# Optimization experiments

Hardware: AMD Instinct MI355X
Metric: run time of the kernel (lower is better)

The kernel has to match this reference:

```python
import jax, jax.numpy as jnp
import numpy as np

N = 65536  # number of points
# (out_ch, in_ch) for the 8 shared-MLP (1x1-conv) blocks
_DIMS = [(64, 3), (64, 64), (128, 64), (1024, 128), (512, 1088), (256, 512), (128, 256), (1, 128)]


def setup_inputs() -> dict:
    key = jax.random.key(0)
    ks = jax.random.split(key, 1 + 2 * len(_DIMS))
    inp = {"x": jax.random.normal(ks[0], (1, 1, N, 3), jnp.float32)}
    for i, (o, c) in enumerate(_DIMS):
        scale = 1.0 / np.sqrt(c)
        inp[f"W{i+1}"] = jax.random.normal(ks[1 + 2 * i], (o, c), jnp.float32) * scale
        inp[f"b{i+1}"] = jax.random.uniform(ks[2 + 2 * i], (o,), jnp.float32, -scale, scale)
    return inp


def reference(x, W1, b1, W2, b2, W3, b3, W4, b4, W5, b5, W6, b6, W7, b7, W8, b8):
    # x: [1,1,n,3]. Conv2d with kernel [1,3] over the width-3 axis == per-point linear on xyz.
    pts = x[0, 0]                                   # [n,3]
    n = pts.shape[0]
    h = jax.nn.relu(pts @ W1.T + b1)                # [n,64]   block1
    h = jax.nn.relu(h @ W2.T + b2)                  # [n,64]   block2 (kept for skip-concat)
    y = jax.nn.relu(h @ W3.T + b3)                  # [n,128]  block3
    y = jax.nn.relu(y @ W4.T + b4)                  # [n,1024] block4
    g = jnp.max(y, axis=0)                          # [1024]   global max-pool over points
    # broadcast global feature to every point and concat with per-point features -> [n,1088]
    feat = jnp.concatenate([h, jnp.broadcast_to(g, (n, g.shape[0]))], axis=1)
    z = jax.nn.relu(feat @ W5.T + b5)               # [n,512]
    z = jax.nn.relu(z @ W6.T + b6)                  # [n,256]
    z = jax.nn.relu(z @ W7.T + b7)                  # [n,128]
    z = z @ W8.T + b8                               # [n,1]    block8 (no relu)
    return z.reshape(1, 1, n, 1)
```

## Files before the change

kernel.cpp:

```cpp
#include <hip/hip_runtime.h>

#define NPTS 65536

typedef __bf16 bf16_t;
typedef __bf16 bf16x8 __attribute__((ext_vector_type(8)));
typedef float f32x16 __attribute__((ext_vector_type(16)));

#define MFMA32(A, B, C) __builtin_amdgcn_mfma_f32_32x32x16_bf16(A, B, C, 0, 0, 0)

__device__ __forceinline__ float relu(float v) { return v > 0.f ? v : 0.f; }


struct PrepSeg { const float* src; bf16_t* h; bf16_t* l; int SW; int K; int nblk; };
struct PrepAll { PrepSeg seg[6]; };

__global__ __launch_bounds__(256) void kprep(PrepAll pa) {
  int blk = blockIdx.x, i = 0;
  while (blk >= pa.seg[i].nblk) { blk -= pa.seg[i].nblk; ++i; }
  const PrepSeg sg = pa.seg[i];
  int t8 = blk * 256 + threadIdx.x;
  int l = t8 & 63;
  int rest = t8 >> 6;
  int NKC = sg.K >> 4;
  int kc = rest % NKC, st = rest / NKC;
  int n = st * 32 + (l & 31);
  int k0 = kc * 16 + (l >> 5) * 8;
  const float* src = sg.src + (size_t)n * sg.SW + k0;
  bf16x8 hv, lv;
#pragma unroll
  for (int j = 0; j < 8; ++j) {
    float v = src[j];
    bf16_t h = (bf16_t)v;
    hv[j] = h; lv[j] = (bf16_t)(v - (float)h);
  }
  *(bf16x8*)(sg.h + (size_t)t8 * 8) = hv;
  *(bf16x8*)(sg.l + (size_t)t8 * 8) = lv;
}

__global__ __launch_bounds__(256, 2) void k1a(
    const float* __restrict__ x, const float* __restrict__ W1, const float* __restrict__ b1,
    bf16_t* __restrict__ h1h, bf16_t* __restrict__ h1l) {
  int p = blockIdx.x * 256 + threadIdx.x;
  float x0 = x[p * 3 + 0], x1 = x[p * 3 + 1], x2 = x[p * 3 + 2];
  int b = p >> 7, mi = (p >> 5) & 3, p31 = p & 31;
#pragma unroll
  for (int kc = 0; kc < 4; ++kc)
#pragma unroll
    for (int hbw = 0; hbw < 2; ++hbw) {
      bf16x8 hv, lv;
#pragma unroll
      for (int j = 0; j < 8; ++j) {
        int c = kc * 16 + hbw * 8 + j;
        float v = relu(fmaf(W1[c * 3], x0, fmaf(W1[c * 3 + 1], x1, fmaf(W1[c * 3 + 2], x2, b1[c]))));
        bf16_t h = (bf16_t)v;
        hv[j] = h; lv[j] = (bf16_t)(v - (float)h);
      }
      size_t off = (((size_t)(b * 4 + kc) * 4 + mi) * 64 + hbw * 32 + p31) * 8;
      *(bf16x8*)(h1h + off) = hv;
      *(bf16x8*)(h1l + off) = lv;
    }
}

struct Oct { bf16x8 h0, l0, h1, l1; };
__device__ __forceinline__ Oct epi_pack(const f32x16& accv, int hb) {
  float a[16], rcv[8];
#pragma unroll
  for (int r = 0; r < 16; ++r) a[r] = relu(accv[r]);
#pragma unroll
  for (int j = 0; j < 8; ++j) rcv[j] = __shfl_xor(hb ? a[j] : a[8 + j], 32);
  float o0[8], o1[8];
#pragma unroll
  for (int j = 0; j < 4; ++j) {
    o0[j]     = hb ? rcv[j]     : a[j];
    o0[4 + j] = hb ? a[8 + j]   : rcv[j];
    o1[j]     = hb ? rcv[4 + j] : a[4 + j];
    o1[4 + j] = hb ? a[12 + j]  : rcv[4 + j];
  }
  Oct o;
#pragma unroll
  for (int j = 0; j < 8; ++j) {
    bf16_t x0 = (bf16_t)o0[j]; o.h0[j] = x0; o.l0[j] = (bf16_t)(o0[j] - (float)x0);
    bf16_t x1 = (bf16_t)o1[j]; o.h1[j] = x1; o.l1[j] = (bf16_t)(o1[j] - (float)x1);
  }
  return o;
}

__device__ __forceinline__ void epi_store_lds(const Oct& o, bf16_t* H, bf16_t* L, int ob, int p31) {
  *(bf16x8*)(H + (ob + p31) * 8)      = o.h0;
  *(bf16x8*)(H + (ob + 32 + p31) * 8) = o.h1;
  *(bf16x8*)(L + (ob + p31) * 8)      = o.l0;
  *(bf16x8*)(L + (ob + 32 + p31) * 8) = o.l1;
}

__device__ __forceinline__ void binit2(f32x16 acc[2], const float* bias, int base, int hb) {
#pragma unroll
  for (int r = 0; r < 16; ++r) {
    float bv = bias[base + 8 * (r >> 2) + 4 * hb + (r & 3)];
    acc[0][r] = bv; acc[1][r] = bv;
  }
}

template <int PB, int K, int MODE>
__global__ __launch_bounds__(256, 3) void gemmS(
    const bf16_t* __restrict__ Ah, const bf16_t* __restrict__ Al,
    const bf16_t* __restrict__ Wh, const bf16_t* __restrict__ Wl,
    const float* __restrict__ bias, int nko,
    bf16_t* __restrict__ Oh, bf16_t* __restrict__ Ol,
    float* __restrict__ aux, const float* __restrict__ w8, const float* __restrict__ b8) {
  constexpr int WC = 4 / PB;
  constexpr int NKC = K / 16;
  constexpr int KG = 2;
  constexpr int NG = NKC / KG;
  __shared__ bf16_t smem[2][PB][2][KG * 2048];

  int tid = threadIdx.x;
  int lane = tid & 63;
  int w = __builtin_amdgcn_readfirstlane(tid >> 6);
  int rg = w / WC, cw = w % WC;
  int hb = lane >> 5, p31 = lane & 31;
  int bx = blockIdx.x;
  int st0 = blockIdx.y * WC + cw;
  int bblk = bx * PB + rg;

  f32x16 acc[4];
#pragma unroll
  for (int r = 0; r < 16; ++r) {
    float bv = bias[st0 * 32 + 8 * (r >> 2) + 4 * hb + (r & 3)];
#pragma unroll
    for (int mi = 0; mi < 4; ++mi) acc[mi][r] = bv;
  }

  auto stage = [&](int buf, int g) {
#pragma unroll
    for (int i = 0; i < PB * 4; ++i) {
      int u = i * 256 + tid;
      int rgs = u >> 10, rem = u & 1023;
      int t = rem >> 9, inner = rem & 511;
      const bf16_t* src = (t ? Al : Ah) +
          ((size_t)(bx * PB + rgs) * NKC + g * KG) * 2048 + inner * 8;
      *(bf16x8*)&smem[buf][rgs][t][inner * 8] = *(const bf16x8*)src;
    }
  };

  bf16x8 wch[KG], wcl[KG], wnh[KG], wnl[KG];
  auto wload = [&](int g, bf16x8* h, bf16x8* l) {
#pragma unroll
    for (int kcl = 0; kcl < KG; ++kcl) {
      size_t wo = (((size_t)st0 * NKC + g * KG + kcl) * 64 + lane) * 8;
      h[kcl] = *(const bf16x8*)(Wh + wo);
      l[kcl] = *(const bf16x8*)(Wl + wo);
    }
  };

  auto compute = [&](int buf, bf16x8* h, bf16x8* l) {
#pragma unroll
    for (int kcl = 0; kcl < KG; ++kcl)
#pragma unroll
      for (int mi = 0; mi < 4; ++mi) {
        const bf16_t* xp = &smem[buf][rg][0][((kcl * 4 + mi) * 64 + lane) * 8];
        bf16x8 xh = *(const bf16x8*)xp;
        bf16x8 xl = *(const bf16x8*)(xp + KG * 2048);
        acc[mi] = MFMA32(h[kcl], xh, acc[mi]);
        acc[mi] = MFMA32(l[kcl], xh, acc[mi]);
        acc[mi] = MFMA32(h[kcl], xl, acc[mi]);
      }
  };

  stage(0, 0);
  wload(0, wch, wcl);
  for (int g = 0; g < NG; ++g) {
    __syncthreads();
    if (g + 1 < NG) {
      stage((g + 1) & 1, g + 1);
      wload(g + 1, wnh, wnl);
    }
    compute(g & 1, wch, wcl);
#pragma unroll
    for (int kcl = 0; kcl < KG; ++kcl) { wch[kcl] = wnh[kcl]; wcl[kcl] = wnl[kcl]; }
  }

  if constexpr (MODE == 0) {
#pragma unroll
    for (int mi = 0; mi < 4; ++mi) {
      Oct o = epi_pack(acc[mi], hb);
      int kco = st0 * 2 + hb;
      size_t ob = ((size_t)(bblk * nko + kco) * 4 + mi) * 64;
      *(bf16x8*)(Oh + (ob + p31) * 8)      = o.h0;
      *(bf16x8*)(Ol + (ob + p31) * 8)      = o.l0;
      *(bf16x8*)(Oh + (ob + 32 + p31) * 8) = o.h1;
      *(bf16x8*)(Ol + (ob + 32 + p31) * 8) = o.l1;
    }
  } else if constexpr (MODE == 1) {
#pragma unroll
    for (int r = 0; r < 16; ++r) {
      float m = relu(acc[0][r]);
#pragma unroll
      for (int mi = 1; mi < 4; ++mi) m = fmaxf(m, relu(acc[mi][r]));
#pragma unroll
      for (int off = 1; off < 32; off <<= 1) m = fmaxf(m, __shfl_xor(m, off));
      if (p31 == 0)
        aux[(size_t)bx * 1024 + st0 * 32 + 8 * (r >> 2) + 4 * hb + (r & 3)] = m;
    }
  } else {
    __shared__ float sp[4][128];
    float w8v[16];
#pragma unroll
    for (int r = 0; r < 16; ++r) w8v[r] = w8[st0 * 32 + 8 * (r >> 2) + 4 * hb + (r & 3)];
#pragma unroll
    for (int mi = 0; mi < 4; ++mi) {
      float s = 0.f;
#pragma unroll
      for (int r = 0; r < 16; ++r) s = fmaf(relu(acc[mi][r]), w8v[r], s);
      s += __shfl_xor(s, 32);
      if (hb == 0) sp[w][mi * 32 + p31] = s;
    }
    __syncthreads();
    if (tid < 128)
      aux[(size_t)bx * 128 + tid] = sp[0][tid] + sp[1][tid] + sp[2][tid] + sp[3][tid] + b8[0];
  }
}

__global__ __launch_bounds__(512, 1) void kl34max(
    const bf16_t* __restrict__ h2h, const bf16_t* __restrict__ h2l,
    const bf16_t* __restrict__ W3h, const bf16_t* __restrict__ W3l,
    const float* __restrict__ b3,
    const bf16_t* __restrict__ Wh, const bf16_t* __restrict__ Wl,
    const float* __restrict__ bias, float* __restrict__ gpart) {
  __shared__ __align__(16) bf16_t sA[65536];
  int tid = threadIdx.x, lane = tid & 63;
  int w = __builtin_amdgcn_readfirstlane(tid >> 6);
  int w3 = w & 3, t = w >> 2;
  int hb = lane >> 5, p31 = lane & 31;
  int bx = blockIdx.x;
  int pb = bx * 2 + t;
  int rot = (bx >> 2) & 7;
  bf16_t* sT = sA + t * 32768;

  bf16x8 hx[4], lx[4];
#pragma unroll
  for (int kc = 0; kc < 4; ++kc) {
    size_t so = (((size_t)(pb * 4 + kc) * 4 + w3) * 64 + lane) * 8;
    hx[kc] = *(const bf16x8*)(h2h + so);
    lx[kc] = *(const bf16x8*)(h2l + so);
  }
#pragma unroll
  for (int spr = 0; spr < 2; ++spr) {
    f32x16 a3[2];
#pragma unroll
    for (int s = 0; s < 2; ++s) {
      int st = spr * 2 + s;
#pragma unroll
      for (int r = 0; r < 16; ++r)
        a3[s][r] = b3[st * 32 + 8 * (r >> 2) + 4 * hb + (r & 3)];
    }
#pragma unroll
    for (int kc = 0; kc < 4; ++kc)
#pragma unroll
      for (int s = 0; s < 2; ++s) {
        int st = spr * 2 + s;
        size_t wo = ((size_t)(st * 4 + kc) * 64 + lane) * 8;
        bf16x8 wh3 = *(const bf16x8*)(W3h + wo);
        bf16x8 wl3 = *(const bf16x8*)(W3l + wo);
        a3[s] = MFMA32(wh3, hx[kc], a3[s]);
        a3[s] = MFMA32(wl3, hx[kc], a3[s]);
        a3[s] = MFMA32(wh3, lx[kc], a3[s]);
      }
#pragma unroll
    for (int s = 0; s < 2; ++s) {
      int st = spr * 2 + s;
      Oct o = epi_pack(a3[s], hb);
      epi_store_lds(o, sT, sT + 16384, ((st * 2 + hb) * 4 + w3) * 64, p31);
    }
  }
  __syncthreads();

#pragma unroll 1
  for (int j = 0; j < 8; ++j) {
    int st = ((j + rot) & 7) * 4 + w3;
    bf16x8 cwh, cwl, nwh, nwl;
    {
      size_t wo = ((size_t)(st * 8) * 64 + lane) * 8;
      cwh = *(const bf16x8*)(Wh + wo);
      cwl = *(const bf16x8*)(Wl + wo);
    }
    f32x16 acc[4];
#pragma unroll
    for (int r = 0; r < 16; ++r) {
      float bv = bias[st * 32 + 8 * (r >> 2) + 4 * hb + (r & 3)];
#pragma unroll
      for (int mi = 0; mi < 4; ++mi) acc[mi][r] = bv;
    }
#pragma unroll
    for (int kc = 0; kc < 8; ++kc) {
      if (kc < 7) {
        size_t wo = ((size_t)(st * 8 + kc + 1) * 64 + lane) * 8;
        nwh = *(const bf16x8*)(Wh + wo);
        nwl = *(const bf16x8*)(Wl + wo);
      }
      __builtin_amdgcn_s_setprio(1);
#pragma unroll
      for (int mi = 0; mi < 4; ++mi) {
        const bf16_t* xp = sT + ((kc * 4 + mi) * 64 + lane) * 8;
        bf16x8 xh = *(const bf16x8*)xp;
        bf16x8 xl = *(const bf16x8*)(xp + 16384);
        acc[mi] = MFMA32(cwh, xh, acc[mi]);
        acc[mi] = MFMA32(cwl, xh, acc[mi]);
        acc[mi] = MFMA32(cwh, xl, acc[mi]);
      }
      __builtin_amdgcn_s_setprio(0);
      cwh = nwh; cwl = nwl;
    }
#pragma unroll
    for (int r = 0; r < 16; ++r) {
      float m = fmaxf(fmaxf(acc[0][r], acc[1][r]), fmaxf(acc[2][r], acc[3][r]));
      m = fmaxf(m, 0.f);
#pragma unroll
      for (int off = 1; off < 32; off <<= 1) m = fmaxf(m, __shfl_xor(m, off));
      if (p31 == 0)
        __builtin_nontemporal_store(
            m, gpart + (size_t)pb * 1024 + st * 32 + 8 * (r >> 2) + 4 * hb + (r & 3));
    }
  }
}

__global__ __launch_bounds__(256) void kgmax(const float* __restrict__ gpart, float* __restrict__ g) {
  int t = blockIdx.x * 256 + threadIdx.x;
  int c = t & 1023, rg = t >> 10;
  const float* gp = gpart + (size_t)rg * 64 * 1024 + c;
  float m = 0.f;
#pragma unroll 8
  for (int r = 0; r < 64; ++r) m = fmaxf(m, gp[(size_t)r * 1024]);
  atomicMax((unsigned int*)(g + c), __float_as_uint(m));
}

__global__ __launch_bounds__(256) void kc5(
    const float* __restrict__ W5, const float* __restrict__ b5,
    const float* __restrict__ g, float* __restrict__ c5) {
  int tid = threadIdx.x;
  int ci = tid >> 3, kg = tid & 7;
  int c = blockIdx.x * 32 + ci;
  const float* wrow = W5 + (size_t)c * 1088 + 64 + kg * 128;
  const float* gp = g + kg * 128;
  float acc = 0.f;
#pragma unroll 8
  for (int k = 0; k < 128; ++k) acc += wrow[k] * gp[k];
#pragma unroll
  for (int off = 1; off <= 4; off <<= 1) acc += __shfl_xor(acc, off);
  if (kg == 0) c5[c] = acc + b5[c];
}


__global__ __launch_bounds__(256, 2) void mega2(
    const bf16_t* __restrict__ h2gh, const bf16_t* __restrict__ h2gl,
    const bf16_t* __restrict__ W5h, const bf16_t* __restrict__ W5l, const float* __restrict__ c5,
    const bf16_t* __restrict__ W6h, const bf16_t* __restrict__ W6l, const float* __restrict__ b6,
    const bf16_t* __restrict__ W7h, const bf16_t* __restrict__ W7l, const float* __restrict__ b7,
    const float* __restrict__ w8, const float* __restrict__ b8v, float* __restrict__ out) {
  __shared__ __align__(16) bf16_t smem[32768];
  __shared__ float sp[4][64];
  int tid = threadIdx.x, lane = tid & 63;
  int w = __builtin_amdgcn_readfirstlane(tid >> 6);
  int hb = lane >> 5, p31 = lane & 31;
  int b = blockIdx.x;
  int B = b >> 1, half = b & 1;

  bf16x8 xh[4][2], xl[4][2];
#pragma unroll
  for (int kc = 0; kc < 4; ++kc)
#pragma unroll
    for (int mi = 0; mi < 2; ++mi) {
      size_t so = (((size_t)((B * 4 + kc) * 4 + half * 2 + mi)) * 64 + lane) * 8;
      xh[kc][mi] = *(const bf16x8*)(h2gh + so);
      xl[kc][mi] = *(const bf16x8*)(h2gl + so);
    }

  f32x16 z6a[2][2];
#pragma unroll
  for (int s = 0; s < 2; ++s)
#pragma unroll
    for (int r = 0; r < 16; ++r) {
      float bv = b6[(w * 2 + s) * 32 + 8 * (r >> 2) + 4 * hb + (r & 3)];
      z6a[s][0][r] = bv; z6a[s][1][r] = bv;
    }

  bf16x8 w5h[4], w5l[4];
  auto w5load = [&](int g) {
#pragma unroll
    for (int kc = 0; kc < 4; ++kc) {
      size_t wo = (((size_t)(g * 4 + w) * 4 + kc) * 64 + lane) * 8;
      w5h[kc] = *(const bf16x8*)(W5h + wo);
      w5l[kc] = *(const bf16x8*)(W5l + wo);
    }
  };
  w5load(0);

  bf16x8 cwh[2], cwl[2], nwh[2], nwl[2];
  auto w6load = [&](int g, int kc, bf16x8* hh, bf16x8* ll) {
#pragma unroll
    for (int s = 0; s < 2; ++s) {
      size_t wo = ((size_t)((w * 2 + s) * 32 + g * 8 + kc) * 64 + lane) * 8;
      hh[s] = *(const bf16x8*)(W6h + wo);
      ll[s] = *(const bf16x8*)(W6l + wo);
    }
  };

  for (int g5 = 0; g5 < 4; ++g5) {
    bf16_t* zbuf = smem + (g5 & 1) * 16384;
    int st5 = g5 * 4 + w;
    f32x16 a5[2];
    binit2(a5, c5, st5 * 32, hb);
    __builtin_amdgcn_s_setprio(1);
#pragma unroll
    for (int kc = 0; kc < 4; ++kc) {
#pragma unroll
      for (int mi = 0; mi < 2; ++mi) a5[mi] = MFMA32(w5h[kc], xh[kc][mi], a5[mi]);
#pragma unroll
      for (int mi = 0; mi < 2; ++mi) a5[mi] = MFMA32(w5l[kc], xh[kc][mi], a5[mi]);
#pragma unroll
      for (int mi = 0; mi < 2; ++mi) a5[mi] = MFMA32(w5h[kc], xl[kc][mi], a5[mi]);
    }
    __builtin_amdgcn_s_setprio(0);
    if (g5 < 3) w5load(g5 + 1);
#pragma unroll
    for (int mi = 0; mi < 2; ++mi) {
      Oct o = epi_pack(a5[mi], hb);
      epi_store_lds(o, zbuf, zbuf + 8192, ((w * 2 + hb) * 2 + mi) * 64, p31);
    }
    w6load(g5, 0, cwh, cwl);
    __syncthreads();
#pragma unroll
    for (int kc = 0; kc < 8; ++kc) {
      if (kc < 7) w6load(g5, kc + 1, nwh, nwl);
      bf16x8 zxh[2], zxl[2];
#pragma unroll
      for (int mi = 0; mi < 2; ++mi) {
        const bf16_t* xp = zbuf + ((kc * 2 + mi) * 64 + lane) * 8;
        zxh[mi] = *(const bf16x8*)xp;
        zxl[mi] = *(const bf16x8*)(xp + 8192);
      }
      __builtin_amdgcn_s_setprio(1);
#pragma unroll
      for (int s = 0; s < 2; ++s)
#pragma unroll
        for (int mi = 0; mi < 2; ++mi) z6a[s][mi] = MFMA32(cwh[s], zxh[mi], z6a[s][mi]);
#pragma unroll
      for (int s = 0; s < 2; ++s)
#pragma unroll
        for (int mi = 0; mi < 2; ++mi) z6a[s][mi] = MFMA32(cwl[s], zxh[mi], z6a[s][mi]);
#pragma unroll
      for (int s = 0; s < 2; ++s)
#pragma unroll
        for (int mi = 0; mi < 2; ++mi) z6a[s][mi] = MFMA32(cwh[s], zxl[mi], z6a[s][mi]);
      __builtin_amdgcn_s_setprio(0);
#pragma unroll
      for (int s = 0; s < 2; ++s) { cwh[s] = nwh[s]; cwl[s] = nwl[s]; }
    }
  }
  __syncthreads();
#pragma unroll
  for (int s = 0; s < 2; ++s) {
    int kcb = (w * 2 + s) * 2 + hb;
#pragma unroll
    for (int mi = 0; mi < 2; ++mi) {
      Oct o = epi_pack(z6a[s][mi], hb);
      epi_store_lds(o, smem, smem + 16384, (kcb * 2 + mi) * 64, p31);
    }
  }
  bf16x8 a7wh, a7wl, n7h, n7l;
  {
    size_t wo = ((size_t)(w * 16) * 64 + lane) * 8;
    a7wh = *(const bf16x8*)(W7h + wo);
    a7wl = *(const bf16x8*)(W7l + wo);
  }
  __syncthreads();
  f32x16 a7[2];
  binit2(a7, b7, w * 32, hb);
#pragma unroll
  for (int kc = 0; kc < 16; ++kc) {
    if (kc < 15) {
      size_t wo = ((size_t)(w * 16 + kc + 1) * 64 + lane) * 8;
      n7h = *(const bf16x8*)(W7h + wo);
      n7l = *(const bf16x8*)(W7l + wo);
    }
    bf16x8 zxh[2], zxl[2];
#pragma unroll
    for (int mi = 0; mi < 2; ++mi) {
      const bf16_t* xp = smem + ((kc * 2 + mi) * 64 + lane) * 8;
      zxh[mi] = *(const bf16x8*)xp;
      zxl[mi] = *(const bf16x8*)(xp + 16384);
    }
    __builtin_amdgcn_s_setprio(1);
#pragma unroll
    for (int mi = 0; mi < 2; ++mi) a7[mi] = MFMA32(a7wh, zxh[mi], a7[mi]);
#pragma unroll
    for (int mi = 0; mi < 2; ++mi) a7[mi] = MFMA32(a7wl, zxh[mi], a7[mi]);
#pragma unroll
    for (int mi = 0; mi < 2; ++mi) a7[mi] = MFMA32(a7wh, zxl[mi], a7[mi]);
    __builtin_amdgcn_s_setprio(0);
    a7wh = n7h; a7wl = n7l;
  }
  float w8v[16];
#pragma unroll
  for (int r = 0; r < 16; ++r) w8v[r] = w8[w * 32 + 8 * (r >> 2) + 4 * hb + (r & 3)];
#pragma unroll
  for (int mi = 0; mi < 2; ++mi) {
    float s = 0.f;
#pragma unroll
    for (int r = 0; r < 16; ++r) s = fmaf(relu(a7[mi][r]), w8v[r], s);
    s += __shfl_xor(s, 32);
    if (hb == 0) sp[w][mi * 32 + p31] = s;
  }
  __syncthreads();
  if (tid < 64)
    out[b * 64 + tid] = sp[0][tid] + sp[1][tid] + sp[2][tid] + sp[3][tid] + b8v[0];
}

extern "C" void kernel_launch(void* const* d_in, const int* in_sizes, int n_in,
                              void* d_out, int out_size, void* d_ws, size_t ws_size,
                              hipStream_t stream) {
  const float* x  = (const float*)d_in[0];
  const float* W1 = (const float*)d_in[1];  const float* b1 = (const float*)d_in[2];
  const float* W2 = (const float*)d_in[3];  const float* b2 = (const float*)d_in[4];
  const float* W3 = (const float*)d_in[5];  const float* b3 = (const float*)d_in[6];
  const float* W4 = (const float*)d_in[7];  const float* b4 = (const float*)d_in[8];
  const float* W5 = (const float*)d_in[9];  const float* b5 = (const float*)d_in[10];
  const float* W6 = (const float*)d_in[11]; const float* b6 = (const float*)d_in[12];
  const float* W7 = (const float*)d_in[13]; const float* b7 = (const float*)d_in[14];
  const float* W8 = (const float*)d_in[15]; const float* b8 = (const float*)d_in[16];
  float* out = (float*)d_out;

  const size_t MB = 1ull << 20;
  char* ws = (char*)d_ws;
  bf16_t* h2h = (bf16_t*)(ws + 128 * MB);  bf16_t* h2l = (bf16_t*)(ws + 136 * MB);
  bf16_t* h1h = (bf16_t*)(ws + 144 * MB);  bf16_t* h1l = (bf16_t*)(ws + 152 * MB);
  float* gpart = (float*)(ws + 208 * MB);
  float* g     = (float*)(ws + 210 * MB);
  float* c5    = (float*)(ws + 210 * MB + 4096);
  char* wb = ws + 210 * MB + 65536;
  bf16_t* W2h = (bf16_t*)(wb);             bf16_t* W2l = (bf16_t*)(wb + 8192);
  bf16_t* W3h = (bf16_t*)(wb + 16384);     bf16_t* W3l = (bf16_t*)(wb + 32768);
  bf16_t* W4h = (bf16_t*)(wb + 49152);     bf16_t* W4l = (bf16_t*)(wb + 311296);
  bf16_t* W5h = (bf16_t*)(wb + 573440);    bf16_t* W5l = (bf16_t*)(wb + 638976);
  bf16_t* W6h = (bf16_t*)(wb + 704512);    bf16_t* W6l = (bf16_t*)(wb + 966656);
  bf16_t* W7h = (bf16_t*)(wb + 1228800);   bf16_t* W7l = (bf16_t*)(wb + 1294336);

  hipMemsetAsync(g, 0, 1024 * sizeof(float), stream);

  PrepAll pa;
  pa.seg[0] = {W2, W2h, W2l, 64, 64, 2};
  pa.seg[1] = {W3, W3h, W3l, 64, 64, 4};
  pa.seg[2] = {W4, W4h, W4l, 128, 128, 64};
  pa.seg[3] = {W5, W5h, W5l, 1088, 64, 16};
  pa.seg[4] = {W6, W6h, W6l, 512, 512, 64};
  pa.seg[5] = {W7, W7h, W7l, 256, 256, 16};
  kprep<<<166, 256, 0, stream>>>(pa);

  k1a<<<256, 256, 0, stream>>>(x, W1, b1, h1h, h1l);
  gemmS<2, 64, 0><<<dim3(256, 1), 256, 0, stream>>>(
      h1h, h1l, W2h, W2l, b2, 4, h2h, h2l, nullptr, nullptr, nullptr);
  kl34max<<<256, 512, 0, stream>>>(h2h, h2l, W3h, W3l, b3, W4h, W4l, b4, gpart);
  kgmax<<<32, 256, 0, stream>>>(gpart, g);
  kc5<<<16, 256, 0, stream>>>(W5, b5, g, c5);
  mega2<<<1024, 256, 0, stream>>>(h2h, h2l, W5h, W5l, c5, W6h, W6l, b6,
                                  W7h, W7l, b7, W8, b8, out);
}
```

Baseline: 305.5 us.

## Stage layer-4 weights through LDS with async global_load_lds ring buffer

In the fused layer-3/4 max kernel, the per-wave direct global loads of W4 hi/lo fragments are replaced by a 4-slot LDS ring buffer. It is filled with global_load_lds three steps ahead and shared by the two point-tile wave groups. Each weight fragment is now fetched once per block instead of once per wave group, and the load latency is hidden behind MFMA work. The cost is a block-wide barrier every k-step, explicit vmcnt waits, and extra LDS use that grows to 160 KB.

```diff
diff --git a/kernel.cpp b/kernel.cpp
--- a/kernel.cpp
+++ b/kernel.cpp
@@ -226,10 +226,12 @@
     const float* __restrict__ b3,
     const bf16_t* __restrict__ Wh, const bf16_t* __restrict__ Wl,
     const float* __restrict__ bias, float* __restrict__ gpart) {
-  __shared__ __align__(16) bf16_t sA[65536];
+  __shared__ __align__(16) bf16_t sA[81920];
+  bf16_t* wq = sA + 65536;
   int tid = threadIdx.x, lane = tid & 63;
   int w = __builtin_amdgcn_readfirstlane(tid >> 6);
   int w3 = w & 3, t = w >> 2;
+  int sslot = w >> 1, part = w & 1;
   int hb = lane >> 5, p31 = lane & 31;
   int bx = blockIdx.x;
   int pb = bx * 2 + t;
@@ -274,51 +276,62 @@
   }
   __syncthreads();
 
+  auto issueS = [&](int u) {
+    int jj = u >> 3, kc = u & 7;
+    int st = ((jj + rot) & 7) * 4 + sslot;
+    const bf16_t* W = part ? Wl : Wh;
+    const bf16_t* gp = W + ((size_t)(st * 8 + kc) * 64 + lane) * 8;
+    bf16_t* lp = wq + (u & 3) * 4096 + sslot * 1024 + part * 512;
+    __builtin_amdgcn_global_load_lds(
+        (const __attribute__((address_space(1))) void*)gp,
+        (__attribute__((address_space(3))) void*)lp, 16, 0, 0);
+  };
+  issueS(0); issueS(1); issueS(2);
+
+  f32x16 acc[4];
 #pragma unroll 1
-  for (int j = 0; j < 8; ++j) {
-    int st = ((j + rot) & 7) * 4 + w3;
-    bf16x8 cwh, cwl, nwh, nwl;
-    {
-      size_t wo = ((size_t)(st * 8) * 64 + lane) * 8;
-      cwh = *(const bf16x8*)(Wh + wo);
-      cwl = *(const bf16x8*)(Wl + wo);
-    }
-    f32x16 acc[4];
-#pragma unroll
-    for (int r = 0; r < 16; ++r) {
-      float bv = bias[st * 32 + 8 * (r >> 2) + 4 * hb + (r & 3)];
-#pragma unroll
-      for (int mi = 0; mi < 4; ++mi) acc[mi][r] = bv;
-    }
-#pragma unroll
-    for (int kc = 0; kc < 8; ++kc) {
-      if (kc < 7) {
-        size_t wo = ((size_t)(st * 8 + kc + 1) * 64 + lane) * 8;
-        nwh = *(const bf16x8*)(Wh + wo);
-        nwl = *(const bf16x8*)(Wl + wo);
+  for (int u = 0; u < 64; ++u) {
+    if (u <= 61)      asm volatile("s_waitcnt vmcnt(2)" ::: "memory");
+    else if (u == 62) asm volatile("s_waitcnt vmcnt(1)" ::: "memory");
+    else              asm volatile("s_waitcnt vmcnt(0)" ::: "memory");
+    __builtin_amdgcn_sched_barrier(0);
+    __builtin_amdgcn_s_barrier();
+    if (u + 3 < 64) issueS(u + 3);
+    int jj = u >> 3, kc = u & 7;
+    int st = ((jj + rot) & 7) * 4 + w3;
+    if (kc == 0) {
+#pragma unroll
+      for (int r = 0; r < 16; ++r) {
+        float bv = bias[st * 32 + 8 * (r >> 2) + 4 * hb + (r & 3)];
+#pragma unroll
+        for (int mi = 0; mi < 4; ++mi) acc[mi][r] = bv;
       }
-      __builtin_amdgcn_s_setprio(1);
-#pragma unroll
-      for (int mi = 0; mi < 4; ++mi) {
-        const bf16_t* xp = sT + ((kc * 4 + mi) * 64 + lane) * 8;
-        bf16x8 xh = *(const bf16x8*)xp;
-        bf16x8 xl = *(const bf16x8*)(xp + 16384);
-        acc[mi] = MFMA32(cwh, xh, acc[mi]);
-        acc[mi] = MFMA32(cwl, xh, acc[mi]);
-        acc[mi] = MFMA32(cwh, xl, acc[mi]);
+    }
+    const bf16_t* wb = wq + (u & 3) * 4096 + w3 * 1024;
+    bf16x8 cwh = *(const bf16x8*)(wb + lane * 8);
+    bf16x8 cwl = *(const bf16x8*)(wb + 512 + lane * 8);
+    __builtin_amdgcn_s_setprio(1);
+#pragma unroll
+    for (int mi = 0; mi < 4; ++mi) {
+      const bf16_t* xp = sT + ((kc * 4 + mi) * 64 + lane) * 8;
+      bf16x8 xh = *(const bf16x8*)xp;
+      bf16x8 xl = *(const bf16x8*)(xp + 16384);
+      acc[mi] = MFMA32(cwh, xh, acc[mi]);
+      acc[mi] = MFMA32(cwl, xh, acc[mi]);
+      acc[mi] = MFMA32(cwh, xl, acc[mi]);
+    }
+    __builtin_amdgcn_s_setprio(0);
+    if (kc == 7) {
+#pragma unroll
+      for (int r = 0; r < 16; ++r) {
+        float m = fmaxf(fmaxf(acc[0][r], acc[1][r]), fmaxf(acc[2][r], acc[3][r]));
+        m = fmaxf(m, 0.f);
+#pragma unroll
+        for (int off = 1; off < 32; off <<= 1) m = fmaxf(m, __shfl_xor(m, off));
+        if (p31 == 0)
+          __builtin_nontemporal_store(
+              m, gpart + (size_t)pb * 1024 + st * 32 + 8 * (r >> 2) + 4 * hb + (r & 3));
       }
-      __builtin_amdgcn_s_setprio(0);
-      cwh = nwh; cwl = nwl;
-    }
-#pragma unroll
-    for (int r = 0; r < 16; ++r) {
-      float m = fmaxf(fmaxf(acc[0][r], acc[1][r]), fmaxf(acc[2][r], acc[3][r]));
-      m = fmaxf(m, 0.f);
-#pragma unroll
-      for (int off = 1; off < 32; off <<= 1) m = fmaxf(m, __shfl_xor(m, off));
-      if (p31 == 0)
-        __builtin_nontemporal_store(
-            m, gpart + (size_t)pb * 1024 + st * 32 + 8 * (r >> 2) + 4 * hb + (r & 3));
     }
   }
 }
```

Result: faster. 267.0 us (-12.6%).
